# Optimization experiments

Measured on AMD Instinct MI355X. Metric: run time of the kernel, lower is better.

## Reference

```python
import jax, jax.numpy as jnp
import numpy as np

N_NODES = 50000
N_EDGES = 800000
IN_F = 128
HID = 256
N_CLS = 10
NUM_GRAPHS = 256


def setup_inputs() -> dict:
    key = jax.random.key(0)
    ks = jax.random.split(key, 8)
    x = jax.random.normal(ks[0], (N_NODES, IN_F), dtype=jnp.float32)
    edge_index = jax.random.randint(ks[1], (2, N_EDGES), 0, N_NODES, dtype=jnp.int64)
    batch = jnp.sort(jax.random.randint(ks[2], (N_NODES,), 0, NUM_GRAPHS, dtype=jnp.int64))
    # Glorot-style init for weights (GCNConv default), zeros bias
    W1 = jax.random.normal(ks[3], (IN_F, HID), dtype=jnp.float32) / np.sqrt(IN_F)
    b1 = jnp.zeros((HID,), dtype=jnp.float32)
    W2 = jax.random.normal(ks[4], (HID, HID), dtype=jnp.float32) / np.sqrt(HID)
    b2 = jnp.zeros((HID,), dtype=jnp.float32)
    Wlin = jax.random.normal(ks[5], (HID, N_CLS), dtype=jnp.float32) / np.sqrt(HID)
    blin = jnp.zeros((N_CLS,), dtype=jnp.float32)
    return {"x": x, "edge_index": edge_index, "batch": batch,
            "W1": W1, "b1": b1, "W2": W2, "b2": b2, "Wlin": Wlin, "blin": blin}


def reference(x, edge_index, batch, W1, b1, W2, b2, Wlin, blin):
    N = x.shape[0]
    # PyG GCNConv default: add self-loops, symmetric normalization D^-1/2 A D^-1/2
    loop = jnp.arange(N, dtype=edge_index.dtype)
    src = jnp.concatenate([edge_index[0], loop])  # message source (row)
    dst = jnp.concatenate([edge_index[1], loop])  # aggregation target (col)
    deg = jax.ops.segment_sum(jnp.ones_like(dst, dtype=x.dtype), dst, num_segments=N)
    dinv = jnp.where(deg > 0, jax.lax.rsqrt(deg), 0.0)
    norm = dinv[src] * dinv[dst]  # [E+N]

    def gcn_conv(h, W, b):
        h = h @ W                          # linear transform first (GCNConv)
        msg = h[src] * norm[:, None]       # gather + edge scale
        agg = jax.ops.segment_sum(msg, dst, num_segments=N)  # scatter-add
        return agg + b

    h = jax.nn.relu(gcn_conv(x, W1, b1))
    h = gcn_conv(h, W2, b2)

    # global_mean_pool over batch ids
    counts = jax.ops.segment_sum(jnp.ones((N,), x.dtype), batch, num_segments=NUM_GRAPHS)
    pooled = jax.ops.segment_sum(h, batch, num_segments=NUM_GRAPHS)
    pooled = pooled / jnp.maximum(counts, 1.0)[:, None]  # [NUM_GRAPHS, HID]

    return pooled @ Wlin + blin  # forward returns logits (softmax unused in forward)
```

## Files before the change

### kernel.cpp

```cpp
#include <hip/hip_runtime.h>
#include <hip/hip_bf16.h>

typedef __hip_bfloat16 bf16;
typedef __attribute__((ext_vector_type(8))) short short8;
typedef __attribute__((ext_vector_type(4))) float f32x4;
typedef __attribute__((ext_vector_type(2))) float f32x2;

#define N_NODES 50000
#define N_EDGES 800000
#define IN_F    128
#define HID     256
#define N_CLS   10
#define N_GRAPH 256

#define NB 98
#define PBLOCKS 256

__device__ __forceinline__ int IG(const int* __restrict__ p, int i, int w) {
    return w ? p[2 * i] : p[i];
}
__device__ __forceinline__ float LF(const void* __restrict__ p, int i, int isbf) {
    return isbf ? __bfloat162float(((const bf16*)p)[i]) : ((const float*)p)[i];
}
__device__ __forceinline__ float b2f(unsigned short h) {
    union { unsigned u; float f; } c; c.u = ((unsigned)h) << 16; return c.f;
}
__device__ __forceinline__ unsigned short f2b(float x) {
    bf16 h = __float2bfloat16(x);
    union { bf16 b; unsigned short u; } c; c.b = h; return c.u;
}
__device__ __forceinline__ float f8s(unsigned b) {
    union { unsigned u; float f; } c;
    c.u = ((b & 0x80u) << 24) | ((b & 0x7Fu) << 20);
    return c.f;
}
#define F8SCALE 0x1p120f
__device__ __forceinline__ unsigned f2fp8(float x) {
    unsigned short h = f2b(x * 0x1p-120f);
    unsigned s = ((unsigned)h >> 8) & 0x80u;
    unsigned mag = (unsigned)h & 0x7FFFu;
    unsigned r = (mag + 7u + ((mag >> 4) & 1u)) >> 4;
    if (r > 0x7Eu) r = 0x7Eu;
    return s | r;
}

#if defined(__has_builtin)
#if __has_builtin(__builtin_amdgcn_cvt_pk_f32_fp8)
#define HW_FP8 1
#endif
#if __has_builtin(__builtin_amdgcn_cvt_pk_fp8_f32)
#define HW_FP8E 1
#endif
#endif

__device__ __forceinline__ f32x2 cvt2lo(unsigned v) {
#ifdef HW_FP8
    return __builtin_amdgcn_cvt_pk_f32_fp8((int)v, false);
#else
    f32x2 r; r[0] = f8s(v & 0xFF) * F8SCALE; r[1] = f8s((v >> 8) & 0xFF) * F8SCALE; return r;
#endif
}
__device__ __forceinline__ f32x2 cvt2hi(unsigned v) {
#ifdef HW_FP8
    return __builtin_amdgcn_cvt_pk_f32_fp8((int)v, true);
#else
    f32x2 r; r[0] = f8s((v >> 16) & 0xFF) * F8SCALE; r[1] = f8s(v >> 24) * F8SCALE; return r;
#endif
}
__device__ __forceinline__ unsigned pk4_fp8(float v0, float v1, float v2, float v3) {
#ifdef HW_FP8E
    int o = __builtin_amdgcn_cvt_pk_fp8_f32(v0, v1, 0, false);
    o = __builtin_amdgcn_cvt_pk_fp8_f32(v2, v3, o, true);
    return (unsigned)o;
#else
    return f2fp8(v0) | (f2fp8(v1) << 8) | (f2fp8(v2) << 16) | (f2fp8(v3) << 24);
#endif
}

__global__ __launch_bounds__(256) void k_detect(const int* __restrict__ ei,
                                                const unsigned short* __restrict__ x,
                                                int* __restrict__ flags) {
    __shared__ int nz, cnt;
    if (threadIdx.x == 0) { nz = 0; cnt = 0; }
    __syncthreads();
    int found = 0, c = 0;
    for (int s = 0; s < 4; ++s) {
        int idx = 2 * (threadIdx.x * 4 + s) + 1;
        if (ei[idx] != 0) found = 1;
    }
    for (int s = 0; s < 8; ++s) {
        unsigned short h = x[threadIdx.x * 8 + s];
        int e = (h >> 7) & 0xFF;
        if (e >= 110 && e <= 135) c++;
    }
    if (found) atomicAdd(&nz, 1);
    atomicAdd(&cnt, c);
    __syncthreads();
    if (threadIdx.x == 0) {
        flags[0] = (nz == 0) ? 1 : 0;
        flags[1] = (cnt > 1536) ? 1 : 0;
    }
}

__global__ __launch_bounds__(256) void k_partA1(const int* __restrict__ ei, int* __restrict__ bucketCnt,
                                                int* __restrict__ blockBase, const int* __restrict__ flags,
                                                int E, int N) {
    __shared__ int h[NB];
    int t = threadIdx.x;
    if (t < NB) h[t] = 0;
    __syncthreads();
    int w = flags[0];
    for (int e = blockIdx.x * 256 + t; e < E; e += PBLOCKS * 256) {
        int d = IG(ei, E + e, w);
        int s = IG(ei, e, w);
        if ((unsigned)d < (unsigned)N && (unsigned)s < (unsigned)N)
            atomicAdd(&h[d >> 9], 1);
    }
    __syncthreads();
    if (t < NB)
        blockBase[blockIdx.x * NB + t] = atomicAdd(&bucketCnt[t * 16], h[t]);
}

__global__ __launch_bounds__(128) void k_bscan(const int* __restrict__ bucketCnt,
                                               int* __restrict__ bucketBase) {
    __shared__ int s[128];
    int t = threadIdx.x;
    int v = (t < NB) ? bucketCnt[t * 16] : 0;
    s[t] = v;
    __syncthreads();
    for (int off = 1; off < 128; off <<= 1) {
        int add = (t >= off) ? s[t - off] : 0;
        __syncthreads();
        s[t] += add;
        __syncthreads();
    }
    if (t <= NB) bucketBase[t] = (t < NB) ? (s[t] - v) : s[NB - 1] + 0;
    if (t == NB - 1) bucketBase[NB] = s[t];
}

__global__ __launch_bounds__(256) void k_partA2(const int* __restrict__ ei,
                                                const int* __restrict__ bucketBase,
                                                const int* __restrict__ blockBase,
                                                unsigned* __restrict__ part,
                                                const int* __restrict__ flags, int E, int N) {
    __shared__ int cur[NB];
    int t = threadIdx.x;
    if (t < NB) cur[t] = bucketBase[t] + blockBase[blockIdx.x * NB + t];
    __syncthreads();
    int w = flags[0];
    for (int e = blockIdx.x * 256 + t; e < E; e += PBLOCKS * 256) {
        int d = IG(ei, E + e, w);
        int s = IG(ei, e, w);
        if ((unsigned)d < (unsigned)N && (unsigned)s < (unsigned)N) {
            int slot = atomicAdd(&cur[d >> 9], 1);
            part[slot] = ((unsigned)(d & 511) << 16) | (unsigned)s;
        }
    }
}

__global__ __launch_bounds__(256) void k_partB(const unsigned* __restrict__ part,
                                               const int* __restrict__ bucketBase,
                                               int* __restrict__ rowptr, float* __restrict__ dinv,
                                               int* __restrict__ col, int N) {
    __shared__ int hist[512];
    __shared__ int scn[512];
    __shared__ int pair[256];
    int b = blockIdx.x, t = threadIdx.x;
    int s0 = bucketBase[b], e0 = bucketBase[b + 1];
    hist[t] = 0; hist[t + 256] = 0;
    __syncthreads();
    for (int j = s0 + t; j < e0; j += 256)
        atomicAdd(&hist[part[j] >> 16], 1);
    __syncthreads();
    int a0 = hist[2 * t], a1 = hist[2 * t + 1];
    int pv = a0 + a1;
    pair[t] = pv;
    __syncthreads();
    for (int off = 1; off < 256; off <<= 1) {
        int add = (t >= off) ? pair[t - off] : 0;
        __syncthreads();
        pair[t] += add;
        __syncthreads();
    }
    int pbase = pair[t] - pv;
    scn[2 * t] = pbase;
    scn[2 * t + 1] = pbase + a0;
    __syncthreads();
#pragma unroll
    for (int hh = 0; hh < 2; ++hh) {
        int l = t + hh * 256;
        int node = b * 512 + l;
        if (node < N) {
            rowptr[node] = s0 + scn[l];
            dinv[node] = rsqrtf((float)(hist[l] + 1));
        }
    }
    if (b == 0 && t == 0) rowptr[N] = bucketBase[NB];
    __syncthreads();
    for (int j = s0 + t; j < e0; j += 256) {
        unsigned p = part[j];
        int pos = s0 + atomicAdd(&scn[p >> 16], 1);
        col[pos] = (int)(p & 0xFFFFu);
    }
}

#define CVTX_BLOCKS 6250
#define CVT1_BLOCKS 128
#define CVT2_BLOCKS 256
#define GB_BLOCKS   196
__global__ __launch_bounds__(256) void k_cvt(const void* __restrict__ x, const float* __restrict__ dinv,
                                             unsigned char* __restrict__ xs8,
                                             const void* __restrict__ W1, unsigned short* __restrict__ w1t,
                                             const void* __restrict__ W2, unsigned short* __restrict__ w2t,
                                             const int* __restrict__ batch, int* __restrict__ gstart,
                                             const int* __restrict__ flags) {
    int b = blockIdx.x;
    int fb = flags[1];
    if (b < CVTX_BLOCKS) {
        int gid = b * 256 + threadIdx.x;
        int row = gid >> 5;
        float d = dinv[row];
        float vx, vy, vz, vw;
        if (fb) {
            ushort4 v = ((const ushort4*)x)[gid];
            vx = b2f(v.x); vy = b2f(v.y); vz = b2f(v.z); vw = b2f(v.w);
        } else {
            float4 v = ((const float4*)x)[gid];
            vx = v.x; vy = v.y; vz = v.z; vw = v.w;
        }
        ((unsigned*)xs8)[gid] = pk4_fp8(vx * d, vy * d, vz * d, vw * d);
    } else if (b < CVTX_BLOCKS + CVT1_BLOCKS) {
        int i = (b - CVTX_BLOCKS) * 256 + threadIdx.x;
        int n = i >> 7, k = i & 127;
        w1t[i] = f2b(LF(W1, k * 256 + n, fb));
    } else if (b < CVTX_BLOCKS + CVT1_BLOCKS + CVT2_BLOCKS) {
        int i = (b - CVTX_BLOCKS - CVT1_BLOCKS) * 256 + threadIdx.x;
        int n = i >> 8, k = i & 255;
        w2t[i] = f2b(LF(W2, k * 256 + n, fb));
    } else {
        int i = (b - CVTX_BLOCKS - CVT1_BLOCKS - CVT2_BLOCKS) * 256 + threadIdx.x;
        if (i <= N_NODES) {
            int w = flags[0];
            int prev = (i == 0) ? -1 : IG(batch, i - 1, w);
            int cur  = (i == N_NODES) ? N_GRAPH : IG(batch, i, w);
            if (prev < -1) prev = -1;
            if (cur > N_GRAPH) cur = N_GRAPH;
            for (int g = prev + 1; g <= cur; ++g)
                if (g >= 0 && g <= N_GRAPH) gstart[g] = i;
        }
    }
}

__global__ __launch_bounds__(256) void k_gcn2l(const unsigned short* __restrict__ A,
                                               const unsigned short* __restrict__ B1t,
                                               const unsigned short* __restrict__ B2t,
                                               unsigned char* __restrict__ C8, int M,
                                               const float* __restrict__ dinv,
                                               const void* __restrict__ bias1,
                                               const int* __restrict__ flags) {
    __shared__ unsigned short As1[64 * 136];
    __shared__ unsigned short Hs[64 * 264];
    int t = threadIdx.x;
    int lane = t & 63;
    int w = t >> 6;
    int bm = blockIdx.x * 64;
    int l15 = lane & 15, quad = lane >> 4;
    int fb = flags[1];

    {
        const uint4* src = (const uint4*)&A[(size_t)bm * 128];
#pragma unroll
        for (int j = 0; j < 4; ++j) {
            int f = t + j * 256;
            int row = f >> 4, cu = f & 15;
            *(uint4*)&As1[row * 136 + cu * 8] = src[(size_t)row * 16 + cu];
        }
    }
    __syncthreads();

    f32x4 acc[4][4];
#pragma unroll
    for (int ar = 0; ar < 4; ++ar)
#pragma unroll
        for (int tt = 0; tt < 4; ++tt) acc[ar][tt] = (f32x4){0.f, 0.f, 0.f, 0.f};

#pragma unroll
    for (int ks = 0; ks < 4; ++ks) {
        short8 a[4], b[4];
#pragma unroll
        for (int ar = 0; ar < 4; ++ar)
            a[ar] = *(const short8*)&As1[(ar * 16 + l15) * 136 + ks * 32 + quad * 8];
#pragma unroll
        for (int tt = 0; tt < 4; ++tt)
            b[tt] = *(const short8*)&B1t[(size_t)(w * 64 + tt * 16 + l15) * 128 + ks * 32 + quad * 8];
#pragma unroll
        for (int tt = 0; tt < 4; ++tt)
#pragma unroll
            for (int ar = 0; ar < 4; ++ar)
                acc[ar][tt] = __builtin_amdgcn_mfma_f32_16x16x32_bf16(b[tt], a[ar], acc[ar][tt], 0, 0, 0);
    }

    float drow[4];
#pragma unroll
    for (int ar = 0; ar < 4; ++ar) {
        int row = bm + ar * 16 + l15;
        drow[ar] = (row < M) ? dinv[row] : 1.f;
    }
#pragma unroll
    for (int tt = 0; tt < 4; ++tt) {
        int colb = w * 64 + tt * 16 + quad * 4;
        float bc[4];
#pragma unroll
        for (int rr = 0; rr < 4; ++rr) bc[rr] = LF(bias1, colb + rr, fb);
#pragma unroll
        for (int ar = 0; ar < 4; ++ar) {
            ushort4 o;
            o.x = f2b(fmaxf(fmaf(acc[ar][tt][0], drow[ar], bc[0]), 0.f));
            o.y = f2b(fmaxf(fmaf(acc[ar][tt][1], drow[ar], bc[1]), 0.f));
            o.z = f2b(fmaxf(fmaf(acc[ar][tt][2], drow[ar], bc[2]), 0.f));
            o.w = f2b(fmaxf(fmaf(acc[ar][tt][3], drow[ar], bc[3]), 0.f));
            *(ushort4*)&Hs[(ar * 16 + l15) * 264 + colb] = o;
            acc[ar][tt] = (f32x4){0.f, 0.f, 0.f, 0.f};
        }
    }
    __syncthreads();

#pragma unroll
    for (int ks = 0; ks < 8; ++ks) {
        short8 a[4], b[4];
#pragma unroll
        for (int ar = 0; ar < 4; ++ar)
            a[ar] = *(const short8*)&Hs[(ar * 16 + l15) * 264 + ks * 32 + quad * 8];
#pragma unroll
        for (int tt = 0; tt < 4; ++tt)
            b[tt] = *(const short8*)&B2t[(size_t)(w * 64 + tt * 16 + l15) * 256 + ks * 32 + quad * 8];
#pragma unroll
        for (int tt = 0; tt < 4; ++tt)
#pragma unroll
            for (int ar = 0; ar < 4; ++ar)
                acc[ar][tt] = __builtin_amdgcn_mfma_f32_16x16x32_bf16(b[tt], a[ar], acc[ar][tt], 0, 0, 0);
    }

    unsigned* Cs = (unsigned*)As1;
    __syncthreads();
#pragma unroll
    for (int tt = 0; tt < 4; ++tt) {
#pragma unroll
        for (int ar = 0; ar < 4; ++ar) {
            float v0 = acc[ar][tt][0] * drow[ar];
            float v1 = acc[ar][tt][1] * drow[ar];
            float v2 = acc[ar][tt][2] * drow[ar];
            float v3 = acc[ar][tt][3] * drow[ar];
            Cs[(ar * 16 + l15) * 68 + w * 16 + tt * 4 + quad] = pk4_fp8(v0, v1, v2, v3);
        }
    }
    __syncthreads();
    int r = t >> 2, h = t & 3;
    if (bm + r < M) {
        const unsigned* src = Cs + r * 68 + h * 16;
        uint4* dst = (uint4*)&C8[(size_t)(bm + r) * 256 + h * 64];
#pragma unroll
        for (int j = 0; j < 4; ++j) dst[j] = *(const uint4*)(src + j * 4);
    }
}

__global__ __launch_bounds__(256) void k_agg2(const unsigned char* __restrict__ XS,
                                              const int* __restrict__ rowptr, const int* __restrict__ col,
                                              unsigned short* __restrict__ Hout, int N) {
    int jb = blockIdx.x;
    int x8 = jb & 7, k = jb >> 3;
    int gIdx = k >> 4, win = k & 15;
    int node0 = (gIdx * 8 + x8) * 64 + win * 4;
    int lane = threadIdx.x & 63;
    int i = node0 + (threadIdx.x >> 6);
    if (i >= N) return;
    int fo = lane * 2;
    unsigned sv = *(const unsigned short*)&XS[(size_t)i * 128 + fo];
    f32x2 a = cvt2lo(sv);
    int s = rowptr[i], e = rowptr[i + 1];
    int j = s;
    while (j + 16 <= e) {
        unsigned v[16];
#pragma unroll
        for (int q = 0; q < 16; ++q)
            v[q] = *(const unsigned short*)&XS[(size_t)col[j + q] * 128 + fo];
#pragma unroll
        for (int q = 0; q < 16; ++q) a += cvt2lo(v[q]);
        j += 16;
    }
    if (j + 8 <= e) {
        unsigned v[8];
#pragma unroll
        for (int q = 0; q < 8; ++q)
            v[q] = *(const unsigned short*)&XS[(size_t)col[j + q] * 128 + fo];
#pragma unroll
        for (int q = 0; q < 8; ++q) a += cvt2lo(v[q]);
        j += 8;
    }
    if (j + 4 <= e) {
        unsigned v[4];
#pragma unroll
        for (int q = 0; q < 4; ++q)
            v[q] = *(const unsigned short*)&XS[(size_t)col[j + q] * 128 + fo];
#pragma unroll
        for (int q = 0; q < 4; ++q) a += cvt2lo(v[q]);
        j += 4;
    }
    for (; j < e; ++j)
        a += cvt2lo(*(const unsigned short*)&XS[(size_t)col[j] * 128 + fo]);
    ushort2 o;
    o.x = f2b(a[0]); o.y = f2b(a[1]);
    *(ushort2*)&Hout[(size_t)i * 128 + fo] = o;
}

__global__ __launch_bounds__(256) void k_agg4(const unsigned char* __restrict__ XW,
                                              const int* __restrict__ rowptr, const int* __restrict__ col,
                                              const float* __restrict__ dinv, const void* __restrict__ bias,
                                              const int* __restrict__ flags,
                                              unsigned short* __restrict__ Hout, int N) {
    int lane = threadIdx.x & 63;
    int i = (blockIdx.x * 256 + threadIdx.x) >> 6;
    if (i >= N) return;
    int fo = lane * 4;
    unsigned sv = *(const unsigned*)&XW[(size_t)i * 256 + fo];
    f32x2 a01 = cvt2lo(sv), a23 = cvt2hi(sv);
    int s = rowptr[i], e = rowptr[i + 1];
    int j = s;
    while (j + 16 <= e) {
        unsigned v[16];
#pragma unroll
        for (int q = 0; q < 16; ++q)
            v[q] = *(const unsigned*)&XW[(size_t)col[j + q] * 256 + fo];
#pragma unroll
        for (int q = 0; q < 16; ++q) { a01 += cvt2lo(v[q]); a23 += cvt2hi(v[q]); }
        j += 16;
    }
    if (j + 8 <= e) {
        unsigned v[8];
#pragma unroll
        for (int q = 0; q < 8; ++q)
            v[q] = *(const unsigned*)&XW[(size_t)col[j + q] * 256 + fo];
#pragma unroll
        for (int q = 0; q < 8; ++q) { a01 += cvt2lo(v[q]); a23 += cvt2hi(v[q]); }
        j += 8;
    }
    if (j + 4 <= e) {
        unsigned v[4];
#pragma unroll
        for (int q = 0; q < 4; ++q)
            v[q] = *(const unsigned*)&XW[(size_t)col[j + q] * 256 + fo];
#pragma unroll
        for (int q = 0; q < 4; ++q) { a01 += cvt2lo(v[q]); a23 += cvt2hi(v[q]); }
        j += 4;
    }
    for (; j < e; ++j) {
        unsigned v = *(const unsigned*)&XW[(size_t)col[j] * 256 + fo];
        a01 += cvt2lo(v); a23 += cvt2hi(v);
    }
    int fb = flags[1];
    float di = dinv[i];
    float bx = LF(bias, fo + 0, fb), by = LF(bias, fo + 1, fb);
    float bz = LF(bias, fo + 2, fb), bw = LF(bias, fo + 3, fb);
    ushort4 o;
    o.x = f2b(fmaf(a01[0], di, bx)); o.y = f2b(fmaf(a01[1], di, by));
    o.z = f2b(fmaf(a23[0], di, bz)); o.w = f2b(fmaf(a23[1], di, bw));
    *(ushort4*)&Hout[(size_t)i * 256 + fo] = o;
}

__global__ __launch_bounds__(512) void k_poolfinal(const unsigned short* __restrict__ H2,
                                                   const int* __restrict__ gstart,
                                                   const void* __restrict__ Wlin,
                                                   const void* __restrict__ blin,
                                                   const int* __restrict__ flags,
                                                   void* __restrict__ outv) {
    __shared__ float red[8][256];
    __shared__ float p[256];
    int g = blockIdx.x, t = threadIdx.x;
    int sub = t >> 6, lane = t & 63;
    int s = gstart[g], e = gstart[g + 1];
    int cnt = e - s;
    float ax = 0.f, ay = 0.f, az = 0.f, aw = 0.f;
    for (int i = s + sub; i < e; i += 8) {
        ushort4 v = *(const ushort4*)&H2[(size_t)i * 256 + lane * 4];
        ax += b2f(v.x); ay += b2f(v.y); az += b2f(v.z); aw += b2f(v.w);
    }
    red[sub][lane * 4 + 0] = ax;
    red[sub][lane * 4 + 1] = ay;
    red[sub][lane * 4 + 2] = az;
    red[sub][lane * 4 + 3] = aw;
    __syncthreads();
    if (t < 256) {
        float inv = 1.f / fmaxf((float)cnt, 1.f);
        float sum8 = 0.f;
#pragma unroll
        for (int q = 0; q < 8; ++q) sum8 += red[q][t];
        p[t] = sum8 * inv;
    }
    __syncthreads();
    int fb = flags[1];
    if (t < N_CLS) {
        float sum = LF(blin, t, fb);
        for (int f = 0; f < HID; ++f) sum = fmaf(p[f], LF(Wlin, f * N_CLS + t, fb), sum);
        if (fb) ((bf16*)outv)[g * N_CLS + t] = __float2bfloat16(sum);
        else    ((float*)outv)[g * N_CLS + t] = sum;
    }
}

extern "C" void kernel_launch(void* const* d_in, const int* in_sizes, int n_in,
                              void* d_out, int out_size, void* d_ws, size_t ws_size,
                              hipStream_t stream) {
    (void)n_in; (void)ws_size; (void)in_sizes; (void)out_size;
    const void* x     = d_in[0];
    const int*  ei    = (const int*)d_in[1];
    const int*  batch = (const int*)d_in[2];
    const void* W1    = d_in[3];
    const void* b1    = d_in[4];
    const void* W2    = d_in[5];
    const void* b2    = d_in[6];
    const void* Wl    = d_in[7];
    const void* bl    = d_in[8];

    const int N = N_NODES, E = N_EDGES, F = IN_F, H = HID, G = N_GRAPH;

    char* ws = (char*)d_ws;
    size_t off = 0;
    auto alloc = [&](size_t bytes) -> void* {
        void* p = ws + off;
        off += (bytes + 511) & ~(size_t)511;
        return p;
    };
    unsigned char*  xs8  = (unsigned char*)alloc((size_t)N * F);
    unsigned short* aggX = (unsigned short*)alloc((size_t)N * F * 2);
    unsigned char*  XW2s8 = (unsigned char*)alloc((size_t)N * H);
    unsigned short* H2   = (unsigned short*)alloc((size_t)N * H * 2);
    unsigned short* w1t  = (unsigned short*)alloc((size_t)H * F * 2);
    unsigned short* w2t  = (unsigned short*)alloc((size_t)H * H * 2);
    int*   bucketCnt = (int*)alloc((size_t)NB * 16 * 4);
    int*   bucketBase = (int*)alloc((size_t)(NB + 1) * 4);
    int*   blockBase = (int*)alloc((size_t)PBLOCKS * NB * 4);
    unsigned* part  = (unsigned*)alloc((size_t)E * 4);
    int*   gstart  = (int*)alloc((size_t)(G + 1) * 4);
    float* dinv    = (float*)alloc((size_t)N * 4);
    int*   rowptr  = (int*)alloc((size_t)(N + 1) * 4);
    int*   flags   = (int*)alloc(512);
    int*   col     = (int*)alloc((size_t)E * 4);
    size_t zero_bytes = (size_t)NB * 16 * 4;

    hipMemsetAsync(bucketCnt, 0, zero_bytes, stream);

    k_detect<<<1, 256, 0, stream>>>(ei, (const unsigned short*)x, flags);
    k_partA1<<<PBLOCKS, 256, 0, stream>>>(ei, bucketCnt, blockBase, flags, E, N);
    k_bscan<<<1, 128, 0, stream>>>(bucketCnt, bucketBase);
    k_partA2<<<PBLOCKS, 256, 0, stream>>>(ei, bucketBase, blockBase, part, flags, E, N);
    k_partB<<<NB, 256, 0, stream>>>(part, bucketBase, rowptr, dinv, col, N);

    k_cvt<<<CVTX_BLOCKS + CVT1_BLOCKS + CVT2_BLOCKS + GB_BLOCKS, 256, 0, stream>>>(
        x, dinv, xs8, W1, w1t, W2, w2t, batch, gstart, flags);

    int g64 = (N + 63) >> 6;
    int aggBlocks = ((g64 + 7) >> 3) * 8 * 16;
    int nbAgg = (N + 3) / 4;

    k_agg2<<<aggBlocks, 256, 0, stream>>>(xs8, rowptr, col, aggX, N);
    k_gcn2l<<<g64, 256, 0, stream>>>(aggX, w1t, w2t, XW2s8, N, dinv, b1, flags);
    k_agg4<<<nbAgg, 256, 0, stream>>>(XW2s8, rowptr, col, dinv, b2, flags, H2, N);
    k_poolfinal<<<G, 512, 0, stream>>>(H2, gstart, Wl, bl, flags, d_out);
}
```

Measured before the change: 255.2 us.

## Fuse mean-pool partial sums into second aggregation and merge small prep kernels

The second aggregation no longer writes the full bf16 node-feature matrix H2. Each 4-node block sums its rows in shared memory and writes one partial row when all four nodes belong to the same graph, otherwise it atomically adds into a per-graph buffer. The pool kernel then sums the partial rows plus the atomic buffer and adds the bias, which was moved out of the per-node stage. The format detection is folded into k_partA1 as an extra block, and the weight transposes and graph-start computation move into spare blocks of k_partB, removing a launch and shrinking k_cvt. This cuts a large HBM write and reread, at the cost of float atomics and ordering nondeterminism for blocks that straddle graph boundaries.

```diff
diff --git a/kernel.cpp b/kernel.cpp
--- a/kernel.cpp
+++ b/kernel.cpp
@@ -77,39 +77,47 @@
 #endif
 }
 
-__global__ __launch_bounds__(256) void k_detect(const int* __restrict__ ei,
+__global__ __launch_bounds__(256) void k_partA1(const int* __restrict__ ei, int* __restrict__ bucketCnt,
+                                                int* __restrict__ blockBase,
                                                 const unsigned short* __restrict__ x,
-                                                int* __restrict__ flags) {
-    __shared__ int nz, cnt;
-    if (threadIdx.x == 0) { nz = 0; cnt = 0; }
-    __syncthreads();
-    int found = 0, c = 0;
+                                                int* __restrict__ flags, int E, int N) {
+    int t = threadIdx.x;
+    if (blockIdx.x == PBLOCKS) {
+        __shared__ int nz, cnt;
+        if (t == 0) { nz = 0; cnt = 0; }
+        __syncthreads();
+        int found = 0, c = 0;
+        for (int s = 0; s < 4; ++s) {
+            int idx = 2 * (t * 4 + s) + 1;
+            if (ei[idx] != 0) found = 1;
+        }
+        for (int s = 0; s < 8; ++s) {
+            unsigned short h = x[t * 8 + s];
+            int e = (h >> 7) & 0xFF;
+            if (e >= 110 && e <= 135) c++;
+        }
+        if (found) atomicAdd(&nz, 1);
+        atomicAdd(&cnt, c);
+        __syncthreads();
+        if (t == 0) {
+            flags[0] = (nz == 0) ? 1 : 0;
+            flags[1] = (cnt > 1536) ? 1 : 0;
+        }
+        return;
+    }
+    __shared__ int h[NB];
+    __shared__ int wsh;
+    if (t == 0) wsh = 0;
+    if (t < NB) h[t] = 0;
+    __syncthreads();
+    int found = 0;
     for (int s = 0; s < 4; ++s) {
-        int idx = 2 * (threadIdx.x * 4 + s) + 1;
+        int idx = 2 * (t * 4 + s) + 1;
         if (ei[idx] != 0) found = 1;
     }
-    for (int s = 0; s < 8; ++s) {
-        unsigned short h = x[threadIdx.x * 8 + s];
-        int e = (h >> 7) & 0xFF;
-        if (e >= 110 && e <= 135) c++;
-    }
-    if (found) atomicAdd(&nz, 1);
-    atomicAdd(&cnt, c);
-    __syncthreads();
-    if (threadIdx.x == 0) {
-        flags[0] = (nz == 0) ? 1 : 0;
-        flags[1] = (cnt > 1536) ? 1 : 0;
-    }
-}
-
-__global__ __launch_bounds__(256) void k_partA1(const int* __restrict__ ei, int* __restrict__ bucketCnt,
-                                                int* __restrict__ blockBase, const int* __restrict__ flags,
-                                                int E, int N) {
-    __shared__ int h[NB];
-    int t = threadIdx.x;
-    if (t < NB) h[t] = 0;
-    __syncthreads();
-    int w = flags[0];
+    if (found) atomicAdd(&wsh, 1);
+    __syncthreads();
+    int w = (wsh == 0) ? 1 : 0;
     for (int e = blockIdx.x * 256 + t; e < E; e += PBLOCKS * 256) {
         int d = IG(ei, E + e, w);
         int s = IG(ei, e, w);
@@ -158,14 +166,46 @@
     }
 }
 
+#define PB_W1 98
+#define PB_W2 226
+#define PB_GB 482
+#define PB_TOT 678
 __global__ __launch_bounds__(256) void k_partB(const unsigned* __restrict__ part,
                                                const int* __restrict__ bucketBase,
                                                int* __restrict__ rowptr, float* __restrict__ dinv,
-                                               int* __restrict__ col, int N) {
+                                               int* __restrict__ col,
+                                               const void* __restrict__ W1, unsigned short* __restrict__ w1t,
+                                               const void* __restrict__ W2, unsigned short* __restrict__ w2t,
+                                               const int* __restrict__ batch, int* __restrict__ gstart,
+                                               const int* __restrict__ flags, int N) {
+    int b = blockIdx.x, t = threadIdx.x;
+    if (b >= NB) {
+        int fb = flags[1];
+        if (b < PB_W2) {
+            int i = (b - PB_W1) * 256 + t;
+            int n = i >> 7, k = i & 127;
+            w1t[i] = f2b(LF(W1, k * 256 + n, fb));
+        } else if (b < PB_GB) {
+            int i = (b - PB_W2) * 256 + t;
+            int n = i >> 8, k = i & 255;
+            w2t[i] = f2b(LF(W2, k * 256 + n, fb));
+        } else {
+            int i = (b - PB_GB) * 256 + t;
+            if (i <= N_NODES) {
+                int w = flags[0];
+                int prev = (i == 0) ? -1 : IG(batch, i - 1, w);
+                int cur  = (i == N_NODES) ? N_GRAPH : IG(batch, i, w);
+                if (prev < -1) prev = -1;
+                if (cur > N_GRAPH) cur = N_GRAPH;
+                for (int g = prev + 1; g <= cur; ++g)
+                    if (g >= 0 && g <= N_GRAPH) gstart[g] = i;
+            }
+        }
+        return;
+    }
     __shared__ int hist[512];
     __shared__ int scn[512];
     __shared__ int pair[256];
-    int b = blockIdx.x, t = threadIdx.x;
     int s0 = bucketBase[b], e0 = bucketBase[b + 1];
     hist[t] = 0; hist[t + 256] = 0;
     __syncthreads();
@@ -205,50 +245,22 @@
 }
 
 #define CVTX_BLOCKS 6250
-#define CVT1_BLOCKS 128
-#define CVT2_BLOCKS 256
-#define GB_BLOCKS   196
 __global__ __launch_bounds__(256) void k_cvt(const void* __restrict__ x, const float* __restrict__ dinv,
                                              unsigned char* __restrict__ xs8,
-                                             const void* __restrict__ W1, unsigned short* __restrict__ w1t,
-                                             const void* __restrict__ W2, unsigned short* __restrict__ w2t,
-                                             const int* __restrict__ batch, int* __restrict__ gstart,
                                              const int* __restrict__ flags) {
-    int b = blockIdx.x;
     int fb = flags[1];
-    if (b < CVTX_BLOCKS) {
-        int gid = b * 256 + threadIdx.x;
-        int row = gid >> 5;
-        float d = dinv[row];
-        float vx, vy, vz, vw;
-        if (fb) {
-            ushort4 v = ((const ushort4*)x)[gid];
-            vx = b2f(v.x); vy = b2f(v.y); vz = b2f(v.z); vw = b2f(v.w);
-        } else {
-            float4 v = ((const float4*)x)[gid];
-            vx = v.x; vy = v.y; vz = v.z; vw = v.w;
-        }
-        ((unsigned*)xs8)[gid] = pk4_fp8(vx * d, vy * d, vz * d, vw * d);
-    } else if (b < CVTX_BLOCKS + CVT1_BLOCKS) {
-        int i = (b - CVTX_BLOCKS) * 256 + threadIdx.x;
-        int n = i >> 7, k = i & 127;
-        w1t[i] = f2b(LF(W1, k * 256 + n, fb));
-    } else if (b < CVTX_BLOCKS + CVT1_BLOCKS + CVT2_BLOCKS) {
-        int i = (b - CVTX_BLOCKS - CVT1_BLOCKS) * 256 + threadIdx.x;
-        int n = i >> 8, k = i & 255;
-        w2t[i] = f2b(LF(W2, k * 256 + n, fb));
+    int gid = blockIdx.x * 256 + threadIdx.x;
+    int row = gid >> 5;
+    float d = dinv[row];
+    float vx, vy, vz, vw;
+    if (fb) {
+        ushort4 v = ((const ushort4*)x)[gid];
+        vx = b2f(v.x); vy = b2f(v.y); vz = b2f(v.z); vw = b2f(v.w);
     } else {
-        int i = (b - CVTX_BLOCKS - CVT1_BLOCKS - CVT2_BLOCKS) * 256 + threadIdx.x;
-        if (i <= N_NODES) {
-            int w = flags[0];
-            int prev = (i == 0) ? -1 : IG(batch, i - 1, w);
-            int cur  = (i == N_NODES) ? N_GRAPH : IG(batch, i, w);
-            if (prev < -1) prev = -1;
-            if (cur > N_GRAPH) cur = N_GRAPH;
-            for (int g = prev + 1; g <= cur; ++g)
-                if (g >= 0 && g <= N_GRAPH) gstart[g] = i;
-        }
-    }
+        float4 v = ((const float4*)x)[gid];
+        vx = v.x; vy = v.y; vz = v.z; vw = v.w;
+    }
+    ((unsigned*)xs8)[gid] = pk4_fp8(vx * d, vy * d, vz * d, vw * d);
 }
 
 __global__ __launch_bounds__(256) void k_gcn2l(const unsigned short* __restrict__ A,
@@ -413,62 +425,81 @@
     *(ushort2*)&Hout[(size_t)i * 128 + fo] = o;
 }
 
-__global__ __launch_bounds__(256) void k_agg4(const unsigned char* __restrict__ XW,
-                                              const int* __restrict__ rowptr, const int* __restrict__ col,
-                                              const float* __restrict__ dinv, const void* __restrict__ bias,
-                                              const int* __restrict__ flags,
-                                              unsigned short* __restrict__ Hout, int N) {
-    int lane = threadIdx.x & 63;
-    int i = (blockIdx.x * 256 + threadIdx.x) >> 6;
-    if (i >= N) return;
+__global__ __launch_bounds__(256) void k_agg4p(const unsigned char* __restrict__ XW,
+                                               const int* __restrict__ rowptr, const int* __restrict__ col,
+                                               const float* __restrict__ dinv,
+                                               const int* __restrict__ batch,
+                                               const int* __restrict__ flags,
+                                               float* __restrict__ partial,
+                                               float* __restrict__ pooledX, int N) {
+    __shared__ float red[4][256];
+    __shared__ int gs[4];
+    int t = threadIdx.x;
+    int lane = t & 63, sub = t >> 6;
+    int i = blockIdx.x * 4 + sub;
     int fo = lane * 4;
-    unsigned sv = *(const unsigned*)&XW[(size_t)i * 256 + fo];
-    f32x2 a01 = cvt2lo(sv), a23 = cvt2hi(sv);
-    int s = rowptr[i], e = rowptr[i + 1];
-    int j = s;
-    while (j + 16 <= e) {
-        unsigned v[16];
-#pragma unroll
-        for (int q = 0; q < 16; ++q)
-            v[q] = *(const unsigned*)&XW[(size_t)col[j + q] * 256 + fo];
-#pragma unroll
-        for (int q = 0; q < 16; ++q) { a01 += cvt2lo(v[q]); a23 += cvt2hi(v[q]); }
-        j += 16;
-    }
-    if (j + 8 <= e) {
-        unsigned v[8];
-#pragma unroll
-        for (int q = 0; q < 8; ++q)
-            v[q] = *(const unsigned*)&XW[(size_t)col[j + q] * 256 + fo];
-#pragma unroll
-        for (int q = 0; q < 8; ++q) { a01 += cvt2lo(v[q]); a23 += cvt2hi(v[q]); }
-        j += 8;
-    }
-    if (j + 4 <= e) {
-        unsigned v[4];
-#pragma unroll
-        for (int q = 0; q < 4; ++q)
-            v[q] = *(const unsigned*)&XW[(size_t)col[j + q] * 256 + fo];
-#pragma unroll
-        for (int q = 0; q < 4; ++q) { a01 += cvt2lo(v[q]); a23 += cvt2hi(v[q]); }
-        j += 4;
-    }
-    for (; j < e; ++j) {
-        unsigned v = *(const unsigned*)&XW[(size_t)col[j] * 256 + fo];
-        a01 += cvt2lo(v); a23 += cvt2hi(v);
-    }
-    int fb = flags[1];
-    float di = dinv[i];
-    float bx = LF(bias, fo + 0, fb), by = LF(bias, fo + 1, fb);
-    float bz = LF(bias, fo + 2, fb), bw = LF(bias, fo + 3, fb);
-    ushort4 o;
-    o.x = f2b(fmaf(a01[0], di, bx)); o.y = f2b(fmaf(a01[1], di, by));
-    o.z = f2b(fmaf(a23[0], di, bz)); o.w = f2b(fmaf(a23[1], di, bw));
-    *(ushort4*)&Hout[(size_t)i * 256 + fo] = o;
-}
-
-__global__ __launch_bounds__(512) void k_poolfinal(const unsigned short* __restrict__ H2,
+    float v[4] = {0.f, 0.f, 0.f, 0.f};
+    int g = -1;
+    if (i < N) {
+        g = IG(batch, i, flags[0]);
+        unsigned sv = *(const unsigned*)&XW[(size_t)i * 256 + fo];
+        f32x2 a01 = cvt2lo(sv), a23 = cvt2hi(sv);
+        int s = rowptr[i], e = rowptr[i + 1];
+        int j = s;
+        while (j + 16 <= e) {
+            unsigned vv[16];
+#pragma unroll
+            for (int q = 0; q < 16; ++q)
+                vv[q] = *(const unsigned*)&XW[(size_t)col[j + q] * 256 + fo];
+#pragma unroll
+            for (int q = 0; q < 16; ++q) { a01 += cvt2lo(vv[q]); a23 += cvt2hi(vv[q]); }
+            j += 16;
+        }
+        if (j + 8 <= e) {
+            unsigned vv[8];
+#pragma unroll
+            for (int q = 0; q < 8; ++q)
+                vv[q] = *(const unsigned*)&XW[(size_t)col[j + q] * 256 + fo];
+#pragma unroll
+            for (int q = 0; q < 8; ++q) { a01 += cvt2lo(vv[q]); a23 += cvt2hi(vv[q]); }
+            j += 8;
+        }
+        if (j + 4 <= e) {
+            unsigned vv[4];
+#pragma unroll
+            for (int q = 0; q < 4; ++q)
+                vv[q] = *(const unsigned*)&XW[(size_t)col[j + q] * 256 + fo];
+#pragma unroll
+            for (int q = 0; q < 4; ++q) { a01 += cvt2lo(vv[q]); a23 += cvt2hi(vv[q]); }
+            j += 4;
+        }
+        for (; j < e; ++j) {
+            unsigned vv = *(const unsigned*)&XW[(size_t)col[j] * 256 + fo];
+            a01 += cvt2lo(vv); a23 += cvt2hi(vv);
+        }
+        float di = dinv[i];
+        v[0] = a01[0] * di; v[1] = a01[1] * di;
+        v[2] = a23[0] * di; v[3] = a23[1] * di;
+    }
+    if (lane == 0) gs[sub] = g;
+#pragma unroll
+    for (int k2 = 0; k2 < 4; ++k2) red[sub][fo + k2] = v[k2];
+    __syncthreads();
+    bool uni = (gs[0] >= 0) && gs[0] == gs[1] && gs[1] == gs[2] && gs[2] == gs[3];
+    if (uni) {
+        float s4 = red[0][t] + red[1][t] + red[2][t] + red[3][t];
+        partial[(size_t)blockIdx.x * 256 + t] = s4;
+    } else if (g >= 0) {
+#pragma unroll
+        for (int k2 = 0; k2 < 4; ++k2)
+            atomicAdd(&pooledX[g * 256 + fo + k2], v[k2]);
+    }
+}
+
+__global__ __launch_bounds__(512) void k_poolfinal(const float* __restrict__ partial,
+                                                   const float* __restrict__ pooledX,
                                                    const int* __restrict__ gstart,
+                                                   const void* __restrict__ b2,
                                                    const void* __restrict__ Wlin,
                                                    const void* __restrict__ blin,
                                                    const int* __restrict__ flags,
@@ -479,25 +510,28 @@
     int sub = t >> 6, lane = t & 63;
     int s = gstart[g], e = gstart[g + 1];
     int cnt = e - s;
-    float ax = 0.f, ay = 0.f, az = 0.f, aw = 0.f;
-    for (int i = s + sub; i < e; i += 8) {
-        ushort4 v = *(const ushort4*)&H2[(size_t)i * 256 + lane * 4];
-        ax += b2f(v.x); ay += b2f(v.y); az += b2f(v.z); aw += b2f(v.w);
-    }
-    red[sub][lane * 4 + 0] = ax;
-    red[sub][lane * 4 + 1] = ay;
-    red[sub][lane * 4 + 2] = az;
-    red[sub][lane * 4 + 3] = aw;
-    __syncthreads();
+    int b0 = (s + 3) >> 2, b1 = e >> 2;
+    int fo = lane * 4;
+    float a0 = 0.f, a1 = 0.f, a2 = 0.f, a3 = 0.f;
+    for (int b = b0 + sub; b < b1; b += 8) {
+        float4 v = *(const float4*)&partial[(size_t)b * 256 + fo];
+        a0 += v.x; a1 += v.y; a2 += v.z; a3 += v.w;
+    }
+    red[sub][fo + 0] = a0;
+    red[sub][fo + 1] = a1;
+    red[sub][fo + 2] = a2;
+    red[sub][fo + 3] = a3;
+    __syncthreads();
+    int fb = flags[1];
     if (t < 256) {
+        float sum8 = pooledX[g * 256 + t];
+#pragma unroll
+        for (int q = 0; q < 8; ++q) sum8 += red[q][t];
         float inv = 1.f / fmaxf((float)cnt, 1.f);
-        float sum8 = 0.f;
-#pragma unroll
-        for (int q = 0; q < 8; ++q) sum8 += red[q][t];
-        p[t] = sum8 * inv;
-    }
-    __syncthreads();
-    int fb = flags[1];
+        float bb = (cnt > 0) ? LF(b2, t, fb) : 0.f;
+        p[t] = sum8 * inv + bb;
+    }
+    __syncthreads();
     if (t < N_CLS) {
         float sum = LF(blin, t, fb);
         for (int f = 0; f < HID; ++f) sum = fmaf(p[f], LF(Wlin, f * N_CLS + t, fb), sum);
@@ -532,7 +566,8 @@
     unsigned char*  xs8  = (unsigned char*)alloc((size_t)N * F);
     unsigned short* aggX = (unsigned short*)alloc((size_t)N * F * 2);
     unsigned char*  XW2s8 = (unsigned char*)alloc((size_t)N * H);
-    unsigned short* H2   = (unsigned short*)alloc((size_t)N * H * 2);
+    float*          partial = (float*)alloc((size_t)(N / 4) * H * 4);
+    float*          pooledX = (float*)alloc((size_t)G * H * 4);
     unsigned short* w1t  = (unsigned short*)alloc((size_t)H * F * 2);
     unsigned short* w2t  = (unsigned short*)alloc((size_t)H * H * 2);
     int*   bucketCnt = (int*)alloc((size_t)NB * 16 * 4);
@@ -547,15 +582,15 @@
     size_t zero_bytes = (size_t)NB * 16 * 4;
 
     hipMemsetAsync(bucketCnt, 0, zero_bytes, stream);
-
-    k_detect<<<1, 256, 0, stream>>>(ei, (const unsigned short*)x, flags);
-    k_partA1<<<PBLOCKS, 256, 0, stream>>>(ei, bucketCnt, blockBase, flags, E, N);
+    hipMemsetAsync(pooledX, 0, (size_t)G * H * 4, stream);
+
+    k_partA1<<<PBLOCKS + 1, 256, 0, stream>>>(ei, bucketCnt, blockBase,
+                                              (const unsigned short*)x, flags, E, N);
     k_bscan<<<1, 128, 0, stream>>>(bucketCnt, bucketBase);
     k_partA2<<<PBLOCKS, 256, 0, stream>>>(ei, bucketBase, blockBase, part, flags, E, N);
-    k_partB<<<NB, 256, 0, stream>>>(part, bucketBase, rowptr, dinv, col, N);
-
-    k_cvt<<<CVTX_BLOCKS + CVT1_BLOCKS + CVT2_BLOCKS + GB_BLOCKS, 256, 0, stream>>>(
-        x, dinv, xs8, W1, w1t, W2, w2t, batch, gstart, flags);
+    k_partB<<<PB_TOT, 256, 0, stream>>>(part, bucketBase, rowptr, dinv, col,
+                                        W1, w1t, W2, w2t, batch, gstart, flags, N);
+    k_cvt<<<CVTX_BLOCKS, 256, 0, stream>>>(x, dinv, xs8, flags);
 
     int g64 = (N + 63) >> 6;
     int aggBlocks = ((g64 + 7) >> 3) * 8 * 16;
@@ -563,6 +598,6 @@
 
     k_agg2<<<aggBlocks, 256, 0, stream>>>(xs8, rowptr, col, aggX, N);
     k_gcn2l<<<g64, 256, 0, stream>>>(aggX, w1t, w2t, XW2s8, N, dinv, b1, flags);
-    k_agg4<<<nbAgg, 256, 0, stream>>>(XW2s8, rowptr, col, dinv, b2, flags, H2, N);
-    k_poolfinal<<<G, 512, 0, stream>>>(H2, gstart, Wl, bl, flags, d_out);
-}
+    k_agg4p<<<nbAgg, 256, 0, stream>>>(XW2s8, rowptr, col, dinv, batch, flags, partial, pooledX, N);
+    k_poolfinal<<<G, 512, 0, stream>>>(partial, pooledX, gstart, b2, Wl, bl, flags, d_out);
+}
```

Result: no change. 251.7 us (-1.4%).
